# Kernel optimization log

Measured on AMD Instinct MI355X. Metric: run time of the kernel, lower is better.

The kernel has to match this reference:

```python
import jax, jax.numpy as jnp
import numpy as np
import math

B, L, D, H, NT, T, NLAYERS = 64, 128, 512, 8, 10000, 65536, 2
DH = D // H
FF = 2 * D
EPS = 1e-5


def setup_inputs() -> dict:
    key = jax.random.key(0)
    ks = jax.random.split(key, 20)
    item_ids = jax.random.randint(ks[0], (T,), 0, NT, dtype=jnp.int32)
    seg_ids = jnp.sort(jax.random.randint(ks[1], (T,), 0, B * L, dtype=jnp.int32))
    pad_mask = jnp.zeros((B, L), dtype=bool)
    future_mask = jnp.where(jnp.triu(jnp.ones((L, L), dtype=bool), k=1), -1e9, 0.0).astype(jnp.float32)

    s = 0.02
    emb = (jax.random.normal(ks[2], (NT + 1, D), jnp.float32) * s).at[NT].set(0.0)  # padding_idx row is zero
    Wqkv = jax.random.normal(ks[3], (NLAYERS, 3 * D, D), jnp.float32) * s
    bqkv = jnp.zeros((NLAYERS, 3 * D), jnp.float32)
    Wo = jax.random.normal(ks[4], (NLAYERS, D, D), jnp.float32) * s
    bo = jnp.zeros((NLAYERS, D), jnp.float32)
    W1 = jax.random.normal(ks[5], (NLAYERS, FF, D), jnp.float32) * s
    b1 = jnp.zeros((NLAYERS, FF), jnp.float32)
    W2 = jax.random.normal(ks[6], (NLAYERS, D, FF), jnp.float32) * s
    b2 = jnp.zeros((NLAYERS, D), jnp.float32)
    ln1_s = jnp.ones((NLAYERS, D), jnp.float32)
    ln1_b = jnp.zeros((NLAYERS, D), jnp.float32)
    ln2_s = jnp.ones((NLAYERS, D), jnp.float32)
    ln2_b = jnp.zeros((NLAYERS, D), jnp.float32)
    Wout = jax.random.normal(ks[7], (NT, D), jnp.float32) * s
    bout = jnp.zeros((NT,), jnp.float32)
    return dict(item_ids=item_ids, seg_ids=seg_ids, pad_mask=pad_mask, future_mask=future_mask,
                max_len=L, emb=emb, Wqkv=Wqkv, bqkv=bqkv, Wo=Wo, bo=bo, W1=W1, b1=b1, W2=W2, b2=b2,
                ln1_s=ln1_s, ln1_b=ln1_b, ln2_s=ln2_s, ln2_b=ln2_b, Wout=Wout, bout=bout)


def _layernorm(x, s, b):
    m = jnp.mean(x, axis=-1, keepdims=True)
    v = jnp.mean(jnp.square(x - m), axis=-1, keepdims=True)
    return (x - m) * jax.lax.rsqrt(v + EPS) * s + b


def _pos_encoding(maxlen, d):
    den = jnp.exp(-jnp.arange(0, d, 2, dtype=jnp.float32) * (math.log(10000.0) / d))
    pos = jnp.arange(maxlen, dtype=jnp.float32)[:, None]
    pe = jnp.zeros((maxlen, d), jnp.float32)
    pe = pe.at[:, 0::2].set(jnp.sin(pos * den))
    pe = pe.at[:, 1::2].set(jnp.cos(pos * den))
    return pe


def reference(item_ids, seg_ids, pad_mask, future_mask, max_len, emb,
              Wqkv, bqkv, Wo, bo, W1, b1, W2, b2, ln1_s, ln1_b, ln2_s, ln2_b, Wout, bout):
    # fused gather + segment-mean (replaces the per-user Python loops)
    counts = jax.ops.segment_sum(jnp.ones((T,), jnp.float32), seg_ids, num_segments=B * max_len)
    sums = jax.ops.segment_sum(emb[item_ids], seg_ids, num_segments=B * max_len)  # [B*L, D]
    means = jnp.where(counts[:, None] > 0, sums / jnp.maximum(counts, 1.0)[:, None], 0.0)
    x = means.reshape(B, max_len, D) + _pos_encoding(max_len, D)

    key_mask = jnp.where(pad_mask[:, None, None, :], -1e9, 0.0)  # [B,1,1,L]
    scale = 1.0 / math.sqrt(DH)
    for i in range(NLAYERS):
        qkv = x @ Wqkv[i].T + bqkv[i]                         # [B,L,3D]
        q, k, v = jnp.split(qkv, 3, axis=-1)
        q = q.reshape(B, max_len, H, DH)
        k = k.reshape(B, max_len, H, DH)
        v = v.reshape(B, max_len, H, DH)
        scores = jnp.einsum('bqhd,bkhd->bhqk', q, k) * scale + future_mask + key_mask
        attn = jax.nn.softmax(scores, axis=-1)
        o = jnp.einsum('bhqk,bkhd->bqhd', attn, v).reshape(B, max_len, D)
        o = o @ Wo[i].T + bo[i]
        x = _layernorm(x + o, ln1_s[i], ln1_b[i])              # post-norm
        ff = jax.nn.relu(x @ W1[i].T + b1[i]) @ W2[i].T + b2[i]
        x = _layernorm(x + ff, ln2_s[i], ln2_b[i])
    return x @ Wout.T + bout  # [B, L, num_types]
```

## Files before the change

kernel.cpp:

```cpp
#include <hip/hip_runtime.h>

#define T_TOTAL 65536
#define SEQ 128
#define DMODEL 512
#define DHEAD 64
#define NTYPES 10000
#define ROWS 8192
#define NOUT_PAD 10240

typedef float floatx4 __attribute__((ext_vector_type(4)));
typedef short shortx8 __attribute__((ext_vector_type(8)));

#define GLOAD_LDS(gp, lp) __builtin_amdgcn_global_load_lds( \
    (const __attribute__((address_space(1))) void*)(gp),    \
    (__attribute__((address_space(3))) void*)(lp), 16, 0, 0)

#define MFMA_BF16 __builtin_amdgcn_mfma_f32_16x16x32_bf16

__device__ __forceinline__ unsigned short f2bf(float f) {
  union { float f; unsigned u; } v; v.f = f;
  unsigned u = v.u + 0x7fffu + ((v.u >> 16) & 1u);
  return (unsigned short)(u >> 16);
}

__device__ __forceinline__ void phase_barrier() {
  __builtin_amdgcn_sched_barrier(0);
  __builtin_amdgcn_s_barrier();
  __builtin_amdgcn_sched_barrier(0);
}

__global__ __launch_bounds__(256) void convert_pad_kernel(
    const float* __restrict__ src, unsigned short* __restrict__ dst,
    long nsrc, long ndst) {
  long i = (long)blockIdx.x * 1024 + (long)threadIdx.x * 4;
  if (i >= ndst) return;
  float4 v = make_float4(0.f, 0.f, 0.f, 0.f);
  if (i < nsrc) v = *(const float4*)(src + i);
  ushort4 o;
  o.x = f2bf(v.x); o.y = f2bf(v.y); o.z = f2bf(v.z); o.w = f2bf(v.w);
  *(ushort4*)(dst + i) = o;
}

__global__ __launch_bounds__(128) void seg_mean_kernel(
    const int* __restrict__ item_ids, const int* __restrict__ seg_ids,
    const float* __restrict__ emb, float* __restrict__ x_f,
    unsigned short* __restrict__ x_b) {
  int s = blockIdx.x;
  int lo = 0, hi = T_TOTAL;
  while (lo < hi) { int mid = (lo + hi) >> 1; if (seg_ids[mid] < s) lo = mid + 1; else hi = mid; }
  int start = lo;
  hi = T_TOTAL;
  while (lo < hi) { int mid = (lo + hi) >> 1; if (seg_ids[mid] <= s) lo = mid + 1; else hi = mid; }
  int end = lo;
  int c = threadIdx.x << 2;
  float4 acc = make_float4(0.f, 0.f, 0.f, 0.f);
  for (int j = start; j < end; ++j) {
    const float* e = emb + (long)item_ids[j] * DMODEL + c;
    float4 v = *(const float4*)e;
    acc.x += v.x; acc.y += v.y; acc.z += v.z; acc.w += v.w;
  }
  int cnt = end - start;
  float inv = cnt > 0 ? 1.0f / (float)cnt : 0.0f;
  float mv[4] = {acc.x * inv, acc.y * inv, acc.z * inv, acc.w * inv};
  int l = s & (SEQ - 1);
  const float klog = 0.017988946039015984f;
  long base = (long)s * DMODEL + c;
#pragma unroll
  for (int t = 0; t < 4; ++t) {
    int col = c + t;
    float den = expf(-(float)(col & ~1) * klog);
    float ang = (float)l * den;
    float pe = (col & 1) ? cosf(ang) : sinf(ang);
    float val = mv[t] + pe;
    x_f[base + t] = val;
    x_b[base + t] = f2bf(val);
  }
}

__global__ __launch_bounds__(256) void gemm_bt_kernel(
    const unsigned short* __restrict__ A,
    const unsigned short* __restrict__ B,
    const float* __restrict__ bias,
    float* __restrict__ Cf,
    unsigned short* __restrict__ Cb,
    int K, int Nreal, int ldC, int relu) {
  __shared__ unsigned short As[128 * 32];
  __shared__ unsigned short Bs[128 * 32];
  const int tid = threadIdx.x;
  const int lane = tid & 63;
  const int wave = tid >> 6;
  const int wm = (wave >> 1) << 6;
  const int wn = (wave & 1) << 6;
  const int l16 = lane & 15;
  const int quad = lane >> 4;
  const long rowA0 = (long)blockIdx.x * 128;
  const long rowB0 = (long)blockIdx.y * 128;

  floatx4 acc[4][4] = {};

  const int rowOff = tid >> 2;
  const int kOff = (tid & 3) << 3;
  const unsigned short* gA = A + (rowA0 + rowOff) * (long)K + kOff;
  const unsigned short* gB = B + (rowB0 + rowOff) * (long)K + kOff;
  unsigned short* lA = As + tid * 8;
  unsigned short* lB = Bs + tid * 8;

  for (int k0 = 0; k0 < K; k0 += 32) {
    __syncthreads();
    GLOAD_LDS(gA + k0, lA);
    GLOAD_LDS(gA + 64 * (long)K + k0, lA + 2048);
    GLOAD_LDS(gB + k0, lB);
    GLOAD_LDS(gB + 64 * (long)K + k0, lB + 2048);
    __syncthreads();
    shortx8 af[4], bfr[4];
#pragma unroll
    for (int i = 0; i < 4; ++i)
      af[i] = *(const shortx8*)(As + (wm + i * 16 + l16) * 32 + quad * 8);
#pragma unroll
    for (int j = 0; j < 4; ++j)
      bfr[j] = *(const shortx8*)(Bs + (wn + j * 16 + l16) * 32 + quad * 8);
#pragma unroll
    for (int i = 0; i < 4; ++i)
#pragma unroll
      for (int j = 0; j < 4; ++j)
        acc[i][j] = MFMA_BF16(af[i], bfr[j], acc[i][j], 0, 0, 0);
  }

#pragma unroll
  for (int i = 0; i < 4; ++i) {
    int row = (int)rowA0 + wm + i * 16 + quad * 4;
#pragma unroll
    for (int j = 0; j < 4; ++j) {
      int col = (int)rowB0 + wn + j * 16 + l16;
      if (col < Nreal) {
        float bv = bias ? bias[col] : 0.0f;
#pragma unroll
        for (int r = 0; r < 4; ++r) {
          float v = acc[i][j][r] + bv;
          if (relu) v = fmaxf(v, 0.0f);
          long off = (long)(row + r) * ldC + col;
          if (Cf) Cf[off] = v;
          if (Cb) Cb[off] = f2bf(v);
        }
      }
    }
  }
}

__global__ __launch_bounds__(512, 2) void gemm256_kernel(
    const unsigned short* __restrict__ A,
    const unsigned short* __restrict__ B,
    const float* __restrict__ bias,
    float* __restrict__ Cf,
    unsigned short* __restrict__ Cb,
    int K, int Nreal, int ldC, int relu) {
  __shared__ unsigned short As[2][256 * 64];
  __shared__ unsigned short Bs[2][256 * 64];
  const int tid = threadIdx.x;
  const int lane = tid & 63;
  const int wave = tid >> 6;
  const int wm = wave >> 2;
  const int wn = wave & 3;
  const int l16 = lane & 15;
  const int quad = lane >> 4;
  const long rowA0 = (long)blockIdx.x * 256;
  const long rowB0 = (long)blockIdx.y * 256;

  floatx4 acc[8][4] = {};

  const int srow = tid >> 3;
  const int scol = (tid & 7) << 3;
  const unsigned short* gA = A + (rowA0 + srow) * (long)K + scol;
  const unsigned short* gB = B + (rowB0 + srow) * (long)K + scol;
  const int loff = tid * 8;
  const long rstep = 64 * (long)K;

#pragma unroll
  for (int is = 0; is < 4; ++is) {
    GLOAD_LDS(gA + is * rstep, &As[0][is * 4096 + loff]);
    GLOAD_LDS(gB + is * rstep, &Bs[0][is * 4096 + loff]);
  }
  asm volatile("s_waitcnt vmcnt(0)" ::: "memory");
  phase_barrier();

  const int KT = K >> 6;
  for (int kt = 0; kt < KT; ++kt) {
    const int cur = kt & 1;
    const unsigned short* Ab = As[cur];
    const unsigned short* Bb = Bs[cur];
    unsigned short* An = As[cur ^ 1];
    unsigned short* Bn = Bs[cur ^ 1];
    const bool stage = (kt + 1) < KT;
    const unsigned short* gAn = gA + (long)(kt + 1) * 64;
    const unsigned short* gBn = gB + (long)(kt + 1) * 64;

    shortx8 af[4][2], bf[4][2];

#pragma unroll
    for (int m = 0; m < 4; ++m) {
      const unsigned short* p = Ab + (wm * 128 + m * 16 + l16) * 64 + quad * 8;
      af[m][0] = *(const shortx8*)(p);
      af[m][1] = *(const shortx8*)(p + 32);
    }
#pragma unroll
    for (int n = 0; n < 2; ++n) {
      const unsigned short* p = Bb + (wn * 64 + n * 16 + l16) * 64 + quad * 8;
      bf[n][0] = *(const shortx8*)(p);
      bf[n][1] = *(const shortx8*)(p + 32);
    }
    if (stage) {
      GLOAD_LDS(gAn, An + loff);
      GLOAD_LDS(gAn + rstep, An + 4096 + loff);
    }
    phase_barrier();
    __builtin_amdgcn_s_setprio(1);
#pragma unroll
    for (int m = 0; m < 4; ++m)
#pragma unroll
      for (int n = 0; n < 2; ++n) {
        acc[m][n] = MFMA_BF16(af[m][0], bf[n][0], acc[m][n], 0, 0, 0);
        acc[m][n] = MFMA_BF16(af[m][1], bf[n][1], acc[m][n], 0, 0, 0);
      }
    __builtin_amdgcn_s_setprio(0);
    phase_barrier();

#pragma unroll
    for (int n = 2; n < 4; ++n) {
      const unsigned short* p = Bb + (wn * 64 + n * 16 + l16) * 64 + quad * 8;
      bf[n][0] = *(const shortx8*)(p);
      bf[n][1] = *(const shortx8*)(p + 32);
    }
    if (stage) {
      GLOAD_LDS(gAn + 2 * rstep, An + 8192 + loff);
      GLOAD_LDS(gAn + 3 * rstep, An + 12288 + loff);
    }
    phase_barrier();
    __builtin_amdgcn_s_setprio(1);
#pragma unroll
    for (int m = 0; m < 4; ++m)
#pragma unroll
      for (int n = 2; n < 4; ++n) {
        acc[m][n] = MFMA_BF16(af[m][0], bf[n][0], acc[m][n], 0, 0, 0);
        acc[m][n] = MFMA_BF16(af[m][1], bf[n][1], acc[m][n], 0, 0, 0);
      }
    __builtin_amdgcn_s_setprio(0);
    phase_barrier();

#pragma unroll
    for (int m = 0; m < 4; ++m) {
      const unsigned short* p = Ab + (wm * 128 + 64 + m * 16 + l16) * 64 + quad * 8;
      af[m][0] = *(const shortx8*)(p);
      af[m][1] = *(const shortx8*)(p + 32);
    }
    if (stage) {
      GLOAD_LDS(gBn, Bn + loff);
      GLOAD_LDS(gBn + rstep, Bn + 4096 + loff);
    }
    phase_barrier();
    __builtin_amdgcn_s_setprio(1);
#pragma unroll
    for (int m = 0; m < 4; ++m)
#pragma unroll
      for (int n = 0; n < 2; ++n) {
        acc[4 + m][n] = MFMA_BF16(af[m][0], bf[n][0], acc[4 + m][n], 0, 0, 0);
        acc[4 + m][n] = MFMA_BF16(af[m][1], bf[n][1], acc[4 + m][n], 0, 0, 0);
      }
    __builtin_amdgcn_s_setprio(0);
    phase_barrier();

    if (stage) {
      GLOAD_LDS(gBn + 2 * rstep, Bn + 8192 + loff);
      GLOAD_LDS(gBn + 3 * rstep, Bn + 12288 + loff);
    }
    phase_barrier();
    __builtin_amdgcn_s_setprio(1);
#pragma unroll
    for (int m = 0; m < 4; ++m)
#pragma unroll
      for (int n = 2; n < 4; ++n) {
        acc[4 + m][n] = MFMA_BF16(af[m][0], bf[n][0], acc[4 + m][n], 0, 0, 0);
        acc[4 + m][n] = MFMA_BF16(af[m][1], bf[n][1], acc[4 + m][n], 0, 0, 0);
      }
    __builtin_amdgcn_s_setprio(0);
    asm volatile("s_waitcnt vmcnt(0)" ::: "memory");
    phase_barrier();
  }

#pragma unroll
  for (int m = 0; m < 8; ++m) {
    int row = (int)rowA0 + wm * 128 + m * 16 + quad * 4;
#pragma unroll
    for (int n = 0; n < 4; ++n) {
      int col = (int)rowB0 + wn * 64 + n * 16 + l16;
      if (col < Nreal) {
        float bv = bias ? bias[col] : 0.0f;
#pragma unroll
        for (int r = 0; r < 4; ++r) {
          float v = acc[m][n][r] + bv;
          if (relu) v = fmaxf(v, 0.0f);
          long off = (long)(row + r) * ldC + col;
          if (Cf) Cf[off] = v;
          if (Cb) Cb[off] = f2bf(v);
        }
      }
    }
  }
}

__global__ __launch_bounds__(256) void attn_kernel(
    const float* __restrict__ qkv,
    unsigned short* __restrict__ o_b) {
  __shared__ float Ks[SEQ * DHEAD];
  __shared__ float Vs[SEQ * DHEAD];
  __shared__ float Ds[SEQ];
  int b = blockIdx.x >> 3, h = blockIdx.x & 7;
  const float* base = qkv + (long)b * SEQ * 1536;
  int hoff = h * DHEAD;
  for (int idx = threadIdx.x; idx < SEQ * DHEAD; idx += 256) {
    int l = idx >> 6, c = idx & 63;
    Ks[idx] = base[l * 1536 + 512 + hoff + c];
    Vs[idx] = base[l * 1536 + 1024 + hoff + c];
  }
  __syncthreads();
  int l = threadIdx.x & 127;
  int half = threadIdx.x >> 7;
  float q[DHEAD];
#pragma unroll
  for (int c = 0; c < DHEAD; ++c) q[c] = base[l * 1536 + hoff + c];
  float o[DHEAD];
#pragma unroll
  for (int c = 0; c < DHEAD; ++c) o[c] = 0.f;
  float denom = 0.f;
  for (int j = half; j <= l; j += 2) {
    const float* kr = Ks + j * DHEAD;
    float s0 = 0.f, s1 = 0.f, s2 = 0.f, s3 = 0.f;
#pragma unroll
    for (int c = 0; c < DHEAD; c += 4) {
      s0 += q[c] * kr[c];         s1 += q[c + 1] * kr[c + 1];
      s2 += q[c + 2] * kr[c + 2]; s3 += q[c + 3] * kr[c + 3];
    }
    float p = __expf(((s0 + s1) + (s2 + s3)) * 0.125f);
    denom += p;
    const float* vr = Vs + j * DHEAD;
#pragma unroll
    for (int c = 0; c < DHEAD; ++c) o[c] += p * vr[c];
  }
  __syncthreads();
  if (half) {
    float* os = Ks + l * DHEAD;
#pragma unroll
    for (int c = 0; c < DHEAD; ++c) os[c] = o[c];
    Ds[l] = denom;
  }
  __syncthreads();
  if (!half) {
    float dtot = denom + Ds[l];
    float inv = 1.0f / dtot;
    const float* os = Ks + l * DHEAD;
    unsigned short* dst = o_b + ((long)b * SEQ + l) * DMODEL + hoff;
#pragma unroll
    for (int c = 0; c < DHEAD; ++c) dst[c] = f2bf((o[c] + os[c]) * inv);
  }
}

__global__ __launch_bounds__(256) void add_ln_kernel(
    const float* __restrict__ x_in, const float* __restrict__ delta,
    const float* __restrict__ gamma, const float* __restrict__ beta,
    float* __restrict__ x_f, unsigned short* __restrict__ x_b) {
  int row = blockIdx.x;
  int tid = threadIdx.x;
  long base = (long)row * DMODEL;
  int c = tid * 2;
  float2 xv = *(const float2*)(x_in + base + c);
  float2 dv = *(const float2*)(delta + base + c);
  float a = xv.x + dv.x, b = xv.y + dv.y;
  float s = a + b;
  float sq = a * a + b * b;
#pragma unroll
  for (int off = 32; off > 0; off >>= 1) {
    s += __shfl_down(s, off, 64);
    sq += __shfl_down(sq, off, 64);
  }
  __shared__ float red[8];
  __shared__ float mean_s, rstd_s;
  int wv = tid >> 6, ln = tid & 63;
  if (ln == 0) { red[wv] = s; red[4 + wv] = sq; }
  __syncthreads();
  if (tid == 0) {
    float S = red[0] + red[1] + red[2] + red[3];
    float SQ = red[4] + red[5] + red[6] + red[7];
    float mean = S * (1.0f / 512.0f);
    float var = SQ * (1.0f / 512.0f) - mean * mean;
    mean_s = mean;
    rstd_s = rsqrtf(var + 1e-5f);
  }
  __syncthreads();
  float mean = mean_s, rstd = rstd_s;
  float o0 = (a - mean) * rstd * gamma[c] + beta[c];
  float o1 = (b - mean) * rstd * gamma[c + 1] + beta[c + 1];
  x_f[base + c] = o0;
  x_f[base + c + 1] = o1;
  x_b[base + c] = f2bf(o0);
  x_b[base + c + 1] = f2bf(o1);
}

extern "C" void kernel_launch(void* const* d_in, const int* in_sizes, int n_in,
                              void* d_out, int out_size, void* d_ws, size_t ws_size,
                              hipStream_t stream) {
  const int* item_ids = (const int*)d_in[0];
  const int* seg_ids = (const int*)d_in[1];
  const float* emb  = (const float*)d_in[5];
  const float* Wqkv = (const float*)d_in[6];
  const float* bqkv = (const float*)d_in[7];
  const float* Wo   = (const float*)d_in[8];
  const float* bo   = (const float*)d_in[9];
  const float* W1   = (const float*)d_in[10];
  const float* b1   = (const float*)d_in[11];
  const float* W2   = (const float*)d_in[12];
  const float* b2   = (const float*)d_in[13];
  const float* ln1s = (const float*)d_in[14];
  const float* ln1b = (const float*)d_in[15];
  const float* ln2s = (const float*)d_in[16];
  const float* ln2b = (const float*)d_in[17];
  const float* Wout = (const float*)d_in[18];
  const float* bout = (const float*)d_in[19];
  float* out = (float*)d_out;

  char* ws = (char*)d_ws;
  size_t off = 0;
  auto alloc = [&](size_t bytes) {
    void* p = ws + off;
    off += (bytes + 255) & ~(size_t)255;
    return p;
  };
  float* x_f  = (float*)alloc((size_t)ROWS * 512 * 4);
  unsigned short* x_b = (unsigned short*)alloc((size_t)ROWS * 512 * 2);
  float* qkv_f = (float*)alloc((size_t)ROWS * 1536 * 4);
  unsigned short* o_b = (unsigned short*)alloc((size_t)ROWS * 512 * 2);
  float* tmp_f = (float*)alloc((size_t)ROWS * 512 * 4);
  unsigned short* h_b = (unsigned short*)alloc((size_t)ROWS * 1024 * 2);
  unsigned short* wqkv_b = (unsigned short*)alloc((size_t)2 * 1536 * 512 * 2);
  unsigned short* wo_b = (unsigned short*)alloc((size_t)2 * 512 * 512 * 2);
  unsigned short* w1_b = (unsigned short*)alloc((size_t)2 * 1024 * 512 * 2);
  unsigned short* w2_b = (unsigned short*)alloc((size_t)2 * 512 * 1024 * 2);
  unsigned short* wout_b = (unsigned short*)alloc((size_t)NOUT_PAD * 512 * 2);

  auto cvt = [&](const float* src, unsigned short* dst, long nsrc, long ndst) {
    unsigned blocks = (unsigned)((ndst + 1023) / 1024);
    convert_pad_kernel<<<blocks, 256, 0, stream>>>(src, dst, nsrc, ndst);
  };
  cvt(Wqkv, wqkv_b, 2L * 1536 * 512, 2L * 1536 * 512);
  cvt(Wo, wo_b, 2L * 512 * 512, 2L * 512 * 512);
  cvt(W1, w1_b, 2L * 1024 * 512, 2L * 1024 * 512);
  cvt(W2, w2_b, 2L * 512 * 1024, 2L * 512 * 1024);
  cvt(Wout, wout_b, (long)NTYPES * 512, (long)NOUT_PAD * 512);

  seg_mean_kernel<<<ROWS, 128, 0, stream>>>(item_ids, seg_ids, emb, x_f, x_b);

  for (int i = 0; i < 2; ++i) {
    gemm256_kernel<<<dim3(32, 6), 512, 0, stream>>>(
        x_b, wqkv_b + (long)i * 1536 * 512, bqkv + i * 1536,
        qkv_f, nullptr, 512, 1536, 1536, 0);
    attn_kernel<<<512, 256, 0, stream>>>(qkv_f, o_b);
    gemm_bt_kernel<<<dim3(64, 4), 256, 0, stream>>>(
        o_b, wo_b + (long)i * 512 * 512, bo + i * 512,
        tmp_f, nullptr, 512, 512, 512, 0);
    add_ln_kernel<<<ROWS, 256, 0, stream>>>(x_f, tmp_f, ln1s + i * 512, ln1b + i * 512, x_f, x_b);
    gemm_bt_kernel<<<dim3(64, 8), 256, 0, stream>>>(
        x_b, w1_b + (long)i * 1024 * 512, b1 + i * 1024,
        nullptr, h_b, 512, 1024, 1024, 1);
    gemm_bt_kernel<<<dim3(64, 4), 256, 0, stream>>>(
        h_b, w2_b + (long)i * 512 * 1024, b2 + i * 512,
        tmp_f, nullptr, 1024, 512, 512, 0);
    add_ln_kernel<<<ROWS, 256, 0, stream>>>(x_f, tmp_f, ln2s + i * 512, ln2b + i * 512, x_f, x_b);
  }

  gemm256_kernel<<<dim3(32, 40), 512, 0, stream>>>(
      x_b, wout_b, bout, out, nullptr, 512, NTYPES, NTYPES, 0);
}
```

Baseline: 941.9 us.

## Fuse whole forward pass into one persistent cooperative megakernel with grid syncs

Replaces the sequence of separate launches (weight conversion, segment mean, GEMMs, attention, add+layernorm) with one cooperative persistent kernel of 256 blocks that loops over tiles and separates stages with grid-wide syncs. All GEMMs now use the 256x256 tile path, including the smaller ones that previously used 128x128 tiles. Add+layernorm is rewritten as a wave-per-row shuffle reduction with vectorized loads. The aim is to remove launch gaps and tail effects between the many small kernels, at the cost of grid-sync overhead, fewer tiles per GEMM for the small projections, and a fixed grid size that must fit co-resident.

```diff
diff --git a/kernel.cpp b/kernel.cpp
--- a/kernel.cpp
+++ b/kernel.cpp
@@ -1,4 +1,7 @@
 #include <hip/hip_runtime.h>
+#include <hip/hip_cooperative_groups.h>
+
+namespace cg = cooperative_groups;
 
 #define T_TOTAL 65536
 #define SEQ 128
@@ -7,6 +10,9 @@
 #define NTYPES 10000
 #define ROWS 8192
 #define NOUT_PAD 10240
+#define NBLOCKS 256
+#define NTHREADS 512
+#define SH_BYTES 132096
 
 typedef float floatx4 __attribute__((ext_vector_type(4)));
 typedef short shortx8 __attribute__((ext_vector_type(8)));
@@ -29,133 +35,88 @@
   __builtin_amdgcn_sched_barrier(0);
 }
 
-__global__ __launch_bounds__(256) void convert_pad_kernel(
-    const float* __restrict__ src, unsigned short* __restrict__ dst,
-    long nsrc, long ndst) {
-  long i = (long)blockIdx.x * 1024 + (long)threadIdx.x * 4;
-  if (i >= ndst) return;
-  float4 v = make_float4(0.f, 0.f, 0.f, 0.f);
-  if (i < nsrc) v = *(const float4*)(src + i);
-  ushort4 o;
-  o.x = f2bf(v.x); o.y = f2bf(v.y); o.z = f2bf(v.z); o.w = f2bf(v.w);
-  *(ushort4*)(dst + i) = o;
-}
-
-__global__ __launch_bounds__(128) void seg_mean_kernel(
-    const int* __restrict__ item_ids, const int* __restrict__ seg_ids,
-    const float* __restrict__ emb, float* __restrict__ x_f,
-    unsigned short* __restrict__ x_b) {
-  int s = blockIdx.x;
-  int lo = 0, hi = T_TOTAL;
-  while (lo < hi) { int mid = (lo + hi) >> 1; if (seg_ids[mid] < s) lo = mid + 1; else hi = mid; }
-  int start = lo;
-  hi = T_TOTAL;
-  while (lo < hi) { int mid = (lo + hi) >> 1; if (seg_ids[mid] <= s) lo = mid + 1; else hi = mid; }
-  int end = lo;
-  int c = threadIdx.x << 2;
-  float4 acc = make_float4(0.f, 0.f, 0.f, 0.f);
-  for (int j = start; j < end; ++j) {
-    const float* e = emb + (long)item_ids[j] * DMODEL + c;
-    float4 v = *(const float4*)e;
-    acc.x += v.x; acc.y += v.y; acc.z += v.z; acc.w += v.w;
-  }
-  int cnt = end - start;
-  float inv = cnt > 0 ? 1.0f / (float)cnt : 0.0f;
-  float mv[4] = {acc.x * inv, acc.y * inv, acc.z * inv, acc.w * inv};
-  int l = s & (SEQ - 1);
-  const float klog = 0.017988946039015984f;
-  long base = (long)s * DMODEL + c;
-#pragma unroll
-  for (int t = 0; t < 4; ++t) {
-    int col = c + t;
-    float den = expf(-(float)(col & ~1) * klog);
-    float ang = (float)l * den;
-    float pe = (col & 1) ? cosf(ang) : sinf(ang);
-    float val = mv[t] + pe;
-    x_f[base + t] = val;
-    x_b[base + t] = f2bf(val);
-  }
-}
-
-__global__ __launch_bounds__(256) void gemm_bt_kernel(
-    const unsigned short* __restrict__ A,
-    const unsigned short* __restrict__ B,
-    const float* __restrict__ bias,
-    float* __restrict__ Cf,
-    unsigned short* __restrict__ Cb,
-    int K, int Nreal, int ldC, int relu) {
-  __shared__ unsigned short As[128 * 32];
-  __shared__ unsigned short Bs[128 * 32];
-  const int tid = threadIdx.x;
-  const int lane = tid & 63;
-  const int wave = tid >> 6;
-  const int wm = (wave >> 1) << 6;
-  const int wn = (wave & 1) << 6;
-  const int l16 = lane & 15;
-  const int quad = lane >> 4;
-  const long rowA0 = (long)blockIdx.x * 128;
-  const long rowB0 = (long)blockIdx.y * 128;
-
-  floatx4 acc[4][4] = {};
-
-  const int rowOff = tid >> 2;
-  const int kOff = (tid & 3) << 3;
-  const unsigned short* gA = A + (rowA0 + rowOff) * (long)K + kOff;
-  const unsigned short* gB = B + (rowB0 + rowOff) * (long)K + kOff;
-  unsigned short* lA = As + tid * 8;
-  unsigned short* lB = Bs + tid * 8;
-
-  for (int k0 = 0; k0 < K; k0 += 32) {
-    __syncthreads();
-    GLOAD_LDS(gA + k0, lA);
-    GLOAD_LDS(gA + 64 * (long)K + k0, lA + 2048);
-    GLOAD_LDS(gB + k0, lB);
-    GLOAD_LDS(gB + 64 * (long)K + k0, lB + 2048);
-    __syncthreads();
-    shortx8 af[4], bfr[4];
-#pragma unroll
-    for (int i = 0; i < 4; ++i)
-      af[i] = *(const shortx8*)(As + (wm + i * 16 + l16) * 32 + quad * 8);
-#pragma unroll
-    for (int j = 0; j < 4; ++j)
-      bfr[j] = *(const shortx8*)(Bs + (wn + j * 16 + l16) * 32 + quad * 8);
-#pragma unroll
-    for (int i = 0; i < 4; ++i)
-#pragma unroll
-      for (int j = 0; j < 4; ++j)
-        acc[i][j] = MFMA_BF16(af[i], bfr[j], acc[i][j], 0, 0, 0);
-  }
-
-#pragma unroll
-  for (int i = 0; i < 4; ++i) {
-    int row = (int)rowA0 + wm + i * 16 + quad * 4;
-#pragma unroll
-    for (int j = 0; j < 4; ++j) {
-      int col = (int)rowB0 + wn + j * 16 + l16;
-      if (col < Nreal) {
-        float bv = bias ? bias[col] : 0.0f;
-#pragma unroll
-        for (int r = 0; r < 4; ++r) {
-          float v = acc[i][j][r] + bv;
-          if (relu) v = fmaxf(v, 0.0f);
-          long off = (long)(row + r) * ldC + col;
-          if (Cf) Cf[off] = v;
-          if (Cb) Cb[off] = f2bf(v);
-        }
-      }
-    }
-  }
-}
-
-__global__ __launch_bounds__(512, 2) void gemm256_kernel(
-    const unsigned short* __restrict__ A,
-    const unsigned short* __restrict__ B,
-    const float* __restrict__ bias,
-    float* __restrict__ Cf,
-    unsigned short* __restrict__ Cb,
-    int K, int Nreal, int ldC, int relu) {
-  __shared__ unsigned short As[2][256 * 64];
-  __shared__ unsigned short Bs[2][256 * 64];
+struct MegaParams {
+  const int* item_ids; const int* seg_ids;
+  const float* emb;
+  const float* bqkv; const float* bo; const float* b1; const float* b2;
+  const float* ln1s; const float* ln1b; const float* ln2s; const float* ln2b;
+  const float* bout;
+  const float* Wqkv; const float* Wo; const float* W1; const float* W2; const float* Wout;
+  float* out;
+  float* x_f; unsigned short* x_b; float* qkv_f; unsigned short* o_b;
+  float* tmp_f; unsigned short* h_b;
+  unsigned short* wqkv_b; unsigned short* wo_b; unsigned short* w1_b;
+  unsigned short* w2_b; unsigned short* wout_b;
+};
+
+__device__ __forceinline__ void dev_converts(const MegaParams& P) {
+  const long Q0 = 1572864L / 4;
+  const long Q1 = Q0 + 524288L / 4;
+  const long Q2 = Q1 + 1048576L / 4;
+  const long Q3 = Q2 + 1048576L / 4;
+  const long Q4 = Q3 + 5242880L / 4;
+  const long stride = (long)NBLOCKS * NTHREADS;
+  for (long q = (long)blockIdx.x * NTHREADS + threadIdx.x; q < Q4; q += stride) {
+    const float* src; unsigned short* dst; long i; bool guard = false;
+    if (q < Q0)      { src = P.Wqkv; dst = P.wqkv_b; i = q; }
+    else if (q < Q1) { src = P.Wo;   dst = P.wo_b;   i = q - Q0; }
+    else if (q < Q2) { src = P.W1;   dst = P.w1_b;   i = q - Q1; }
+    else if (q < Q3) { src = P.W2;   dst = P.w2_b;   i = q - Q2; }
+    else             { src = P.Wout; dst = P.wout_b; i = q - Q3; guard = true; }
+    long e = i * 4;
+    float4 v = make_float4(0.f, 0.f, 0.f, 0.f);
+    if (!guard || e < 5120000L) v = *(const float4*)(src + e);
+    ushort4 o;
+    o.x = f2bf(v.x); o.y = f2bf(v.y); o.z = f2bf(v.z); o.w = f2bf(v.w);
+    *(ushort4*)(dst + e) = o;
+  }
+}
+
+__device__ __forceinline__ void dev_seg_mean(const MegaParams& P) {
+  int g = threadIdx.x >> 7;
+  int t128 = threadIdx.x & 127;
+  int c = t128 << 2;
+#pragma unroll
+  for (int it = 0; it < 8; ++it) {
+    int s = blockIdx.x * 32 + it * 4 + g;
+    int lo = 0, hi = T_TOTAL;
+    while (lo < hi) { int mid = (lo + hi) >> 1; if (P.seg_ids[mid] < s) lo = mid + 1; else hi = mid; }
+    int start = lo;
+    hi = T_TOTAL;
+    while (lo < hi) { int mid = (lo + hi) >> 1; if (P.seg_ids[mid] <= s) lo = mid + 1; else hi = mid; }
+    int end = lo;
+    float4 acc = make_float4(0.f, 0.f, 0.f, 0.f);
+    for (int j = start; j < end; ++j) {
+      const float* e = P.emb + (long)P.item_ids[j] * DMODEL + c;
+      float4 v = *(const float4*)e;
+      acc.x += v.x; acc.y += v.y; acc.z += v.z; acc.w += v.w;
+    }
+    int cnt = end - start;
+    float inv = cnt > 0 ? 1.0f / (float)cnt : 0.0f;
+    float mv[4] = {acc.x * inv, acc.y * inv, acc.z * inv, acc.w * inv};
+    int l = s & (SEQ - 1);
+    const float klog = 0.017988946039015984f;
+    long base = (long)s * DMODEL + c;
+#pragma unroll
+    for (int t = 0; t < 4; ++t) {
+      int col = c + t;
+      float den = expf(-(float)(col & ~1) * klog);
+      float ang = (float)l * den;
+      float pe = (col & 1) ? cosf(ang) : sinf(ang);
+      float val = mv[t] + pe;
+      P.x_f[base + t] = val;
+      P.x_b[base + t] = f2bf(val);
+    }
+  }
+}
+
+__device__ __forceinline__ void dev_gemm(char* sh,
+    const unsigned short* __restrict__ A, const unsigned short* __restrict__ B,
+    const float* __restrict__ bias, float* __restrict__ Cf,
+    unsigned short* __restrict__ Cb, int K, int Nreal, int ldC, int relu,
+    int tilesX, int tilesY) {
+  unsigned short* AsBase = (unsigned short*)sh;
+  unsigned short* BsBase = (unsigned short*)(sh + 65536);
   const int tid = threadIdx.x;
   const int lane = tid & 63;
   const int wave = tid >> 6;
@@ -163,167 +124,167 @@
   const int wn = wave & 3;
   const int l16 = lane & 15;
   const int quad = lane >> 4;
-  const long rowA0 = (long)blockIdx.x * 256;
-  const long rowB0 = (long)blockIdx.y * 256;
-
-  floatx4 acc[8][4] = {};
-
   const int srow = tid >> 3;
   const int scol = (tid & 7) << 3;
-  const unsigned short* gA = A + (rowA0 + srow) * (long)K + scol;
-  const unsigned short* gB = B + (rowB0 + srow) * (long)K + scol;
   const int loff = tid * 8;
   const long rstep = 64 * (long)K;
-
-#pragma unroll
-  for (int is = 0; is < 4; ++is) {
-    GLOAD_LDS(gA + is * rstep, &As[0][is * 4096 + loff]);
-    GLOAD_LDS(gB + is * rstep, &Bs[0][is * 4096 + loff]);
-  }
-  asm volatile("s_waitcnt vmcnt(0)" ::: "memory");
-  phase_barrier();
-
+  const int nt = tilesX * tilesY;
   const int KT = K >> 6;
-  for (int kt = 0; kt < KT; ++kt) {
-    const int cur = kt & 1;
-    const unsigned short* Ab = As[cur];
-    const unsigned short* Bb = Bs[cur];
-    unsigned short* An = As[cur ^ 1];
-    unsigned short* Bn = Bs[cur ^ 1];
-    const bool stage = (kt + 1) < KT;
-    const unsigned short* gAn = gA + (long)(kt + 1) * 64;
-    const unsigned short* gBn = gB + (long)(kt + 1) * 64;
-
-    shortx8 af[4][2], bf[4][2];
-
-#pragma unroll
-    for (int m = 0; m < 4; ++m) {
-      const unsigned short* p = Ab + (wm * 128 + m * 16 + l16) * 64 + quad * 8;
-      af[m][0] = *(const shortx8*)(p);
-      af[m][1] = *(const shortx8*)(p + 32);
-    }
-#pragma unroll
-    for (int n = 0; n < 2; ++n) {
-      const unsigned short* p = Bb + (wn * 64 + n * 16 + l16) * 64 + quad * 8;
-      bf[n][0] = *(const shortx8*)(p);
-      bf[n][1] = *(const shortx8*)(p + 32);
-    }
-    if (stage) {
-      GLOAD_LDS(gAn, An + loff);
-      GLOAD_LDS(gAn + rstep, An + 4096 + loff);
-    }
-    phase_barrier();
-    __builtin_amdgcn_s_setprio(1);
-#pragma unroll
-    for (int m = 0; m < 4; ++m)
-#pragma unroll
-      for (int n = 0; n < 2; ++n) {
-        acc[m][n] = MFMA_BF16(af[m][0], bf[n][0], acc[m][n], 0, 0, 0);
-        acc[m][n] = MFMA_BF16(af[m][1], bf[n][1], acc[m][n], 0, 0, 0);
-      }
-    __builtin_amdgcn_s_setprio(0);
-    phase_barrier();
-
-#pragma unroll
-    for (int n = 2; n < 4; ++n) {
-      const unsigned short* p = Bb + (wn * 64 + n * 16 + l16) * 64 + quad * 8;
-      bf[n][0] = *(const shortx8*)(p);
-      bf[n][1] = *(const shortx8*)(p + 32);
-    }
-    if (stage) {
-      GLOAD_LDS(gAn + 2 * rstep, An + 8192 + loff);
-      GLOAD_LDS(gAn + 3 * rstep, An + 12288 + loff);
-    }
-    phase_barrier();
-    __builtin_amdgcn_s_setprio(1);
-#pragma unroll
-    for (int m = 0; m < 4; ++m)
-#pragma unroll
-      for (int n = 2; n < 4; ++n) {
-        acc[m][n] = MFMA_BF16(af[m][0], bf[n][0], acc[m][n], 0, 0, 0);
-        acc[m][n] = MFMA_BF16(af[m][1], bf[n][1], acc[m][n], 0, 0, 0);
-      }
-    __builtin_amdgcn_s_setprio(0);
-    phase_barrier();
-
-#pragma unroll
-    for (int m = 0; m < 4; ++m) {
-      const unsigned short* p = Ab + (wm * 128 + 64 + m * 16 + l16) * 64 + quad * 8;
-      af[m][0] = *(const shortx8*)(p);
-      af[m][1] = *(const shortx8*)(p + 32);
-    }
-    if (stage) {
-      GLOAD_LDS(gBn, Bn + loff);
-      GLOAD_LDS(gBn + rstep, Bn + 4096 + loff);
-    }
-    phase_barrier();
-    __builtin_amdgcn_s_setprio(1);
-#pragma unroll
-    for (int m = 0; m < 4; ++m)
-#pragma unroll
-      for (int n = 0; n < 2; ++n) {
-        acc[4 + m][n] = MFMA_BF16(af[m][0], bf[n][0], acc[4 + m][n], 0, 0, 0);
-        acc[4 + m][n] = MFMA_BF16(af[m][1], bf[n][1], acc[4 + m][n], 0, 0, 0);
-      }
-    __builtin_amdgcn_s_setprio(0);
-    phase_barrier();
-
-    if (stage) {
-      GLOAD_LDS(gBn + 2 * rstep, Bn + 8192 + loff);
-      GLOAD_LDS(gBn + 3 * rstep, Bn + 12288 + loff);
-    }
-    phase_barrier();
-    __builtin_amdgcn_s_setprio(1);
-#pragma unroll
-    for (int m = 0; m < 4; ++m)
-#pragma unroll
-      for (int n = 2; n < 4; ++n) {
-        acc[4 + m][n] = MFMA_BF16(af[m][0], bf[n][0], acc[4 + m][n], 0, 0, 0);
-        acc[4 + m][n] = MFMA_BF16(af[m][1], bf[n][1], acc[4 + m][n], 0, 0, 0);
-      }
-    __builtin_amdgcn_s_setprio(0);
+
+  for (int t = blockIdx.x; t < nt; t += NBLOCKS) {
+    int tbx = t % tilesX, tby = t / tilesX;
+    long rowA0 = (long)tbx * 256;
+    long rowB0 = (long)tby * 256;
+    floatx4 acc[8][4] = {};
+    const unsigned short* gA = A + (rowA0 + srow) * (long)K + scol;
+    const unsigned short* gB = B + (rowB0 + srow) * (long)K + scol;
+
+#pragma unroll
+    for (int is = 0; is < 4; ++is) {
+      GLOAD_LDS(gA + is * rstep, AsBase + is * 4096 + loff);
+      GLOAD_LDS(gB + is * rstep, BsBase + is * 4096 + loff);
+    }
     asm volatile("s_waitcnt vmcnt(0)" ::: "memory");
     phase_barrier();
-  }
-
-#pragma unroll
-  for (int m = 0; m < 8; ++m) {
-    int row = (int)rowA0 + wm * 128 + m * 16 + quad * 4;
-#pragma unroll
-    for (int n = 0; n < 4; ++n) {
-      int col = (int)rowB0 + wn * 64 + n * 16 + l16;
-      if (col < Nreal) {
-        float bv = bias ? bias[col] : 0.0f;
-#pragma unroll
-        for (int r = 0; r < 4; ++r) {
-          float v = acc[m][n][r] + bv;
-          if (relu) v = fmaxf(v, 0.0f);
-          long off = (long)(row + r) * ldC + col;
-          if (Cf) Cf[off] = v;
-          if (Cb) Cb[off] = f2bf(v);
+
+    for (int kt = 0; kt < KT; ++kt) {
+      const int cur = kt & 1;
+      const unsigned short* Ab = AsBase + cur * 16384;
+      const unsigned short* Bb = BsBase + cur * 16384;
+      unsigned short* An = AsBase + (cur ^ 1) * 16384;
+      unsigned short* Bn = BsBase + (cur ^ 1) * 16384;
+      const bool stage = (kt + 1) < KT;
+      const unsigned short* gAn = gA + (long)(kt + 1) * 64;
+      const unsigned short* gBn = gB + (long)(kt + 1) * 64;
+
+      shortx8 af[4][2], bf[4][2];
+
+#pragma unroll
+      for (int m = 0; m < 4; ++m) {
+        const unsigned short* p = Ab + (wm * 128 + m * 16 + l16) * 64 + quad * 8;
+        af[m][0] = *(const shortx8*)(p);
+        af[m][1] = *(const shortx8*)(p + 32);
+      }
+#pragma unroll
+      for (int n = 0; n < 2; ++n) {
+        const unsigned short* p = Bb + (wn * 64 + n * 16 + l16) * 64 + quad * 8;
+        bf[n][0] = *(const shortx8*)(p);
+        bf[n][1] = *(const shortx8*)(p + 32);
+      }
+      if (stage) {
+        GLOAD_LDS(gAn, An + loff);
+        GLOAD_LDS(gAn + rstep, An + 4096 + loff);
+        GLOAD_LDS(gAn + 2 * rstep, An + 8192 + loff);
+        GLOAD_LDS(gAn + 3 * rstep, An + 12288 + loff);
+      }
+      phase_barrier();
+      __builtin_amdgcn_s_setprio(1);
+#pragma unroll
+      for (int m = 0; m < 4; ++m)
+#pragma unroll
+        for (int n = 0; n < 2; ++n) {
+          acc[m][n] = MFMA_BF16(af[m][0], bf[n][0], acc[m][n], 0, 0, 0);
+          acc[m][n] = MFMA_BF16(af[m][1], bf[n][1], acc[m][n], 0, 0, 0);
         }
-      }
-    }
-  }
-}
-
-__global__ __launch_bounds__(256) void attn_kernel(
-    const float* __restrict__ qkv,
-    unsigned short* __restrict__ o_b) {
-  __shared__ float Ks[SEQ * DHEAD];
-  __shared__ float Vs[SEQ * DHEAD];
-  __shared__ float Ds[SEQ];
-  int b = blockIdx.x >> 3, h = blockIdx.x & 7;
+      __builtin_amdgcn_s_setprio(0);
+      phase_barrier();
+
+#pragma unroll
+      for (int n = 2; n < 4; ++n) {
+        const unsigned short* p = Bb + (wn * 64 + n * 16 + l16) * 64 + quad * 8;
+        bf[n][0] = *(const shortx8*)(p);
+        bf[n][1] = *(const shortx8*)(p + 32);
+      }
+      if (stage) {
+        GLOAD_LDS(gBn, Bn + loff);
+        GLOAD_LDS(gBn + rstep, Bn + 4096 + loff);
+        GLOAD_LDS(gBn + 2 * rstep, Bn + 8192 + loff);
+        GLOAD_LDS(gBn + 3 * rstep, Bn + 12288 + loff);
+      }
+      phase_barrier();
+      __builtin_amdgcn_s_setprio(1);
+#pragma unroll
+      for (int m = 0; m < 4; ++m)
+#pragma unroll
+        for (int n = 2; n < 4; ++n) {
+          acc[m][n] = MFMA_BF16(af[m][0], bf[n][0], acc[m][n], 0, 0, 0);
+          acc[m][n] = MFMA_BF16(af[m][1], bf[n][1], acc[m][n], 0, 0, 0);
+        }
+      __builtin_amdgcn_s_setprio(0);
+      phase_barrier();
+
+#pragma unroll
+      for (int m = 0; m < 4; ++m) {
+        const unsigned short* p = Ab + (wm * 128 + 64 + m * 16 + l16) * 64 + quad * 8;
+        af[m][0] = *(const shortx8*)(p);
+        af[m][1] = *(const shortx8*)(p + 32);
+      }
+      phase_barrier();
+      __builtin_amdgcn_s_setprio(1);
+#pragma unroll
+      for (int m = 0; m < 4; ++m)
+#pragma unroll
+        for (int n = 0; n < 2; ++n) {
+          acc[4 + m][n] = MFMA_BF16(af[m][0], bf[n][0], acc[4 + m][n], 0, 0, 0);
+          acc[4 + m][n] = MFMA_BF16(af[m][1], bf[n][1], acc[4 + m][n], 0, 0, 0);
+        }
+      __builtin_amdgcn_s_setprio(0);
+      phase_barrier();
+
+      __builtin_amdgcn_s_setprio(1);
+#pragma unroll
+      for (int m = 0; m < 4; ++m)
+#pragma unroll
+        for (int n = 2; n < 4; ++n) {
+          acc[4 + m][n] = MFMA_BF16(af[m][0], bf[n][0], acc[4 + m][n], 0, 0, 0);
+          acc[4 + m][n] = MFMA_BF16(af[m][1], bf[n][1], acc[4 + m][n], 0, 0, 0);
+        }
+      __builtin_amdgcn_s_setprio(0);
+      asm volatile("s_waitcnt vmcnt(0)" ::: "memory");
+      phase_barrier();
+    }
+
+#pragma unroll
+    for (int m = 0; m < 8; ++m) {
+      int row = (int)rowA0 + wm * 128 + m * 16 + quad * 4;
+#pragma unroll
+      for (int n = 0; n < 4; ++n) {
+        int col = (int)rowB0 + wn * 64 + n * 16 + l16;
+        if (col < Nreal) {
+          float bv = bias ? bias[col] : 0.0f;
+#pragma unroll
+          for (int r = 0; r < 4; ++r) {
+            float v = acc[m][n][r] + bv;
+            if (relu) v = fmaxf(v, 0.0f);
+            long off = (long)(row + r) * ldC + col;
+            if (Cf) Cf[off] = v;
+            if (Cb) Cb[off] = f2bf(v);
+          }
+        }
+      }
+    }
+  }
+}
+
+__device__ __forceinline__ void dev_attn(char* sh, const float* __restrict__ qkv,
+                                         unsigned short* __restrict__ o_b) {
+  const int ph = threadIdx.x >> 8;
+  const int t256 = threadIdx.x & 255;
+  float* Ks = (float*)sh + ph * 8192;
+  float* Vs = (float*)(sh + 65536) + ph * 8192;
+  float* Ds = (float*)(sh + 131072) + ph * 128;
+  int p = blockIdx.x * 2 + ph;
+  int b = p >> 3, h = p & 7;
   const float* base = qkv + (long)b * SEQ * 1536;
   int hoff = h * DHEAD;
-  for (int idx = threadIdx.x; idx < SEQ * DHEAD; idx += 256) {
+  for (int idx = t256; idx < SEQ * DHEAD; idx += 256) {
     int l = idx >> 6, c = idx & 63;
     Ks[idx] = base[l * 1536 + 512 + hoff + c];
     Vs[idx] = base[l * 1536 + 1024 + hoff + c];
   }
   __syncthreads();
-  int l = threadIdx.x & 127;
-  int half = threadIdx.x >> 7;
+  int l = t256 & 127;
+  int half = t256 >> 7;
   float q[DHEAD];
 #pragma unroll
   for (int c = 0; c < DHEAD; ++c) q[c] = base[l * 1536 + hoff + c];
@@ -339,11 +300,11 @@
       s0 += q[c] * kr[c];         s1 += q[c + 1] * kr[c + 1];
       s2 += q[c + 2] * kr[c + 2]; s3 += q[c + 3] * kr[c + 3];
     }
-    float p = __expf(((s0 + s1) + (s2 + s3)) * 0.125f);
-    denom += p;
+    float pv = __expf(((s0 + s1) + (s2 + s3)) * 0.125f);
+    denom += pv;
     const float* vr = Vs + j * DHEAD;
 #pragma unroll
-    for (int c = 0; c < DHEAD; ++c) o[c] += p * vr[c];
+    for (int c = 0; c < DHEAD; ++c) o[c] += pv * vr[c];
   }
   __syncthreads();
   if (half) {
@@ -363,69 +324,81 @@
   }
 }
 
-__global__ __launch_bounds__(256) void add_ln_kernel(
-    const float* __restrict__ x_in, const float* __restrict__ delta,
-    const float* __restrict__ gamma, const float* __restrict__ beta,
-    float* __restrict__ x_f, unsigned short* __restrict__ x_b) {
-  int row = blockIdx.x;
-  int tid = threadIdx.x;
-  long base = (long)row * DMODEL;
-  int c = tid * 2;
-  float2 xv = *(const float2*)(x_in + base + c);
-  float2 dv = *(const float2*)(delta + base + c);
-  float a = xv.x + dv.x, b = xv.y + dv.y;
-  float s = a + b;
-  float sq = a * a + b * b;
-#pragma unroll
-  for (int off = 32; off > 0; off >>= 1) {
-    s += __shfl_down(s, off, 64);
-    sq += __shfl_down(sq, off, 64);
-  }
-  __shared__ float red[8];
-  __shared__ float mean_s, rstd_s;
-  int wv = tid >> 6, ln = tid & 63;
-  if (ln == 0) { red[wv] = s; red[4 + wv] = sq; }
-  __syncthreads();
-  if (tid == 0) {
-    float S = red[0] + red[1] + red[2] + red[3];
-    float SQ = red[4] + red[5] + red[6] + red[7];
-    float mean = S * (1.0f / 512.0f);
-    float var = SQ * (1.0f / 512.0f) - mean * mean;
-    mean_s = mean;
-    rstd_s = rsqrtf(var + 1e-5f);
-  }
-  __syncthreads();
-  float mean = mean_s, rstd = rstd_s;
-  float o0 = (a - mean) * rstd * gamma[c] + beta[c];
-  float o1 = (b - mean) * rstd * gamma[c + 1] + beta[c + 1];
-  x_f[base + c] = o0;
-  x_f[base + c + 1] = o1;
-  x_b[base + c] = f2bf(o0);
-  x_b[base + c + 1] = f2bf(o1);
+__device__ __forceinline__ void dev_add_ln(const float* __restrict__ x_in,
+    const float* __restrict__ delta, const float* __restrict__ gamma,
+    const float* __restrict__ beta, float* __restrict__ x_f,
+    unsigned short* __restrict__ x_b) {
+  int w = threadIdx.x >> 6, lane = threadIdx.x & 63;
+  int c = lane * 8;
+#pragma unroll
+  for (int it = 0; it < 4; ++it) {
+    int row = blockIdx.x * 32 + it * 8 + w;
+    long base = (long)row * DMODEL;
+    float4 v0 = *(const float4*)(x_in + base + c);
+    float4 v1 = *(const float4*)(x_in + base + c + 4);
+    float4 d0 = *(const float4*)(delta + base + c);
+    float4 d1 = *(const float4*)(delta + base + c + 4);
+    float e[8] = {v0.x + d0.x, v0.y + d0.y, v0.z + d0.z, v0.w + d0.w,
+                  v1.x + d1.x, v1.y + d1.y, v1.z + d1.z, v1.w + d1.w};
+    float s = 0.f, sq = 0.f;
+#pragma unroll
+    for (int k = 0; k < 8; ++k) { s += e[k]; sq += e[k] * e[k]; }
+#pragma unroll
+    for (int off = 1; off < 64; off <<= 1) {
+      s += __shfl_xor(s, off, 64);
+      sq += __shfl_xor(sq, off, 64);
+    }
+    float mean = s * (1.0f / 512.0f);
+    float var = sq * (1.0f / 512.0f) - mean * mean;
+    float rstd = rsqrtf(var + 1e-5f);
+    float of[8]; unsigned short ob[8];
+#pragma unroll
+    for (int k = 0; k < 8; ++k) {
+      float o = (e[k] - mean) * rstd * gamma[c + k] + beta[c + k];
+      of[k] = o; ob[k] = f2bf(o);
+    }
+    *(float4*)(x_f + base + c) = make_float4(of[0], of[1], of[2], of[3]);
+    *(float4*)(x_f + base + c + 4) = make_float4(of[4], of[5], of[6], of[7]);
+    *(ushort4*)(x_b + base + c) = make_ushort4(ob[0], ob[1], ob[2], ob[3]);
+    *(ushort4*)(x_b + base + c + 4) = make_ushort4(ob[4], ob[5], ob[6], ob[7]);
+  }
+}
+
+__global__ __launch_bounds__(NTHREADS, 2) void mega_kernel(MegaParams P) {
+  __shared__ __attribute__((aligned(128))) char sh[SH_BYTES];
+  cg::grid_group grid = cg::this_grid();
+
+  dev_converts(P);
+  dev_seg_mean(P);
+  grid.sync();
+
+  for (int i = 0; i < 2; ++i) {
+    dev_gemm(sh, P.x_b, P.wqkv_b + (long)i * 1536 * 512, P.bqkv + i * 1536,
+             P.qkv_f, nullptr, 512, 1536, 1536, 0, 32, 6);
+    grid.sync();
+    dev_attn(sh, P.qkv_f, P.o_b);
+    grid.sync();
+    dev_gemm(sh, P.o_b, P.wo_b + (long)i * 512 * 512, P.bo + i * 512,
+             P.tmp_f, nullptr, 512, 512, 512, 0, 32, 2);
+    grid.sync();
+    dev_add_ln(P.x_f, P.tmp_f, P.ln1s + i * 512, P.ln1b + i * 512, P.x_f, P.x_b);
+    grid.sync();
+    dev_gemm(sh, P.x_b, P.w1_b + (long)i * 1024 * 512, P.b1 + i * 1024,
+             nullptr, P.h_b, 512, 1024, 1024, 1, 32, 4);
+    grid.sync();
+    dev_gemm(sh, P.h_b, P.w2_b + (long)i * 512 * 1024, P.b2 + i * 512,
+             P.tmp_f, nullptr, 1024, 512, 512, 0, 32, 2);
+    grid.sync();
+    dev_add_ln(P.x_f, P.tmp_f, P.ln2s + i * 512, P.ln2b + i * 512, P.x_f, P.x_b);
+    grid.sync();
+  }
+
+  dev_gemm(sh, P.x_b, P.wout_b, P.bout, P.out, nullptr, 512, NTYPES, NTYPES, 0, 32, 40);
 }
 
 extern "C" void kernel_launch(void* const* d_in, const int* in_sizes, int n_in,
                               void* d_out, int out_size, void* d_ws, size_t ws_size,
                               hipStream_t stream) {
-  const int* item_ids = (const int*)d_in[0];
-  const int* seg_ids = (const int*)d_in[1];
-  const float* emb  = (const float*)d_in[5];
-  const float* Wqkv = (const float*)d_in[6];
-  const float* bqkv = (const float*)d_in[7];
-  const float* Wo   = (const float*)d_in[8];
-  const float* bo   = (const float*)d_in[9];
-  const float* W1   = (const float*)d_in[10];
-  const float* b1   = (const float*)d_in[11];
-  const float* W2   = (const float*)d_in[12];
-  const float* b2   = (const float*)d_in[13];
-  const float* ln1s = (const float*)d_in[14];
-  const float* ln1b = (const float*)d_in[15];
-  const float* ln2s = (const float*)d_in[16];
-  const float* ln2b = (const float*)d_in[17];
-  const float* Wout = (const float*)d_in[18];
-  const float* bout = (const float*)d_in[19];
-  float* out = (float*)d_out;
-
   char* ws = (char*)d_ws;
   size_t off = 0;
   auto alloc = [&](size_t bytes) {
@@ -433,48 +406,40 @@
     off += (bytes + 255) & ~(size_t)255;
     return p;
   };
-  float* x_f  = (float*)alloc((size_t)ROWS * 512 * 4);
-  unsigned short* x_b = (unsigned short*)alloc((size_t)ROWS * 512 * 2);
-  float* qkv_f = (float*)alloc((size_t)ROWS * 1536 * 4);
-  unsigned short* o_b = (unsigned short*)alloc((size_t)ROWS * 512 * 2);
-  float* tmp_f = (float*)alloc((size_t)ROWS * 512 * 4);
-  unsigned short* h_b = (unsigned short*)alloc((size_t)ROWS * 1024 * 2);
-  unsigned short* wqkv_b = (unsigned short*)alloc((size_t)2 * 1536 * 512 * 2);
-  unsigned short* wo_b = (unsigned short*)alloc((size_t)2 * 512 * 512 * 2);
-  unsigned short* w1_b = (unsigned short*)alloc((size_t)2 * 1024 * 512 * 2);
-  unsigned short* w2_b = (unsigned short*)alloc((size_t)2 * 512 * 1024 * 2);
-  unsigned short* wout_b = (unsigned short*)alloc((size_t)NOUT_PAD * 512 * 2);
-
-  auto cvt = [&](const float* src, unsigned short* dst, long nsrc, long ndst) {
-    unsigned blocks = (unsigned)((ndst + 1023) / 1024);
-    convert_pad_kernel<<<blocks, 256, 0, stream>>>(src, dst, nsrc, ndst);
-  };
-  cvt(Wqkv, wqkv_b, 2L * 1536 * 512, 2L * 1536 * 512);
-  cvt(Wo, wo_b, 2L * 512 * 512, 2L * 512 * 512);
-  cvt(W1, w1_b, 2L * 1024 * 512, 2L * 1024 * 512);
-  cvt(W2, w2_b, 2L * 512 * 1024, 2L * 512 * 1024);
-  cvt(Wout, wout_b, (long)NTYPES * 512, (long)NOUT_PAD * 512);
-
-  seg_mean_kernel<<<ROWS, 128, 0, stream>>>(item_ids, seg_ids, emb, x_f, x_b);
-
-  for (int i = 0; i < 2; ++i) {
-    gemm256_kernel<<<dim3(32, 6), 512, 0, stream>>>(
-        x_b, wqkv_b + (long)i * 1536 * 512, bqkv + i * 1536,
-        qkv_f, nullptr, 512, 1536, 1536, 0);
-    attn_kernel<<<512, 256, 0, stream>>>(qkv_f, o_b);
-    gemm_bt_kernel<<<dim3(64, 4), 256, 0, stream>>>(
-        o_b, wo_b + (long)i * 512 * 512, bo + i * 512,
-        tmp_f, nullptr, 512, 512, 512, 0);
-    add_ln_kernel<<<ROWS, 256, 0, stream>>>(x_f, tmp_f, ln1s + i * 512, ln1b + i * 512, x_f, x_b);
-    gemm_bt_kernel<<<dim3(64, 8), 256, 0, stream>>>(
-        x_b, w1_b + (long)i * 1024 * 512, b1 + i * 1024,
-        nullptr, h_b, 512, 1024, 1024, 1);
-    gemm_bt_kernel<<<dim3(64, 4), 256, 0, stream>>>(
-        h_b, w2_b + (long)i * 512 * 1024, b2 + i * 512,
-        tmp_f, nullptr, 1024, 512, 512, 0);
-    add_ln_kernel<<<ROWS, 256, 0, stream>>>(x_f, tmp_f, ln2s + i * 512, ln2b + i * 512, x_f, x_b);
-  }
-
-  gemm256_kernel<<<dim3(32, 40), 512, 0, stream>>>(
-      x_b, wout_b, bout, out, nullptr, 512, NTYPES, NTYPES, 0);
-}
+
+  MegaParams P;
+  P.item_ids = (const int*)d_in[0];
+  P.seg_ids  = (const int*)d_in[1];
+  P.emb  = (const float*)d_in[5];
+  P.Wqkv = (const float*)d_in[6];
+  P.bqkv = (const float*)d_in[7];
+  P.Wo   = (const float*)d_in[8];
+  P.bo   = (const float*)d_in[9];
+  P.W1   = (const float*)d_in[10];
+  P.b1   = (const float*)d_in[11];
+  P.W2   = (const float*)d_in[12];
+  P.b2   = (const float*)d_in[13];
+  P.ln1s = (const float*)d_in[14];
+  P.ln1b = (const float*)d_in[15];
+  P.ln2s = (const float*)d_in[16];
+  P.ln2b = (const float*)d_in[17];
+  P.Wout = (const float*)d_in[18];
+  P.bout = (const float*)d_in[19];
+  P.out  = (float*)d_out;
+
+  P.x_f    = (float*)alloc((size_t)ROWS * 512 * 4);
+  P.x_b    = (unsigned short*)alloc((size_t)ROWS * 512 * 2);
+  P.qkv_f  = (float*)alloc((size_t)ROWS * 1536 * 4);
+  P.o_b    = (unsigned short*)alloc((size_t)ROWS * 512 * 2);
+  P.tmp_f  = (float*)alloc((size_t)ROWS * 512 * 4);
+  P.h_b    = (unsigned short*)alloc((size_t)ROWS * 1024 * 2);
+  P.wqkv_b = (unsigned short*)alloc((size_t)2 * 1536 * 512 * 2);
+  P.wo_b   = (unsigned short*)alloc((size_t)2 * 512 * 512 * 2);
+  P.w1_b   = (unsigned short*)alloc((size_t)2 * 1024 * 512 * 2);
+  P.w2_b   = (unsigned short*)alloc((size_t)2 * 512 * 1024 * 2);
+  P.wout_b = (unsigned short*)alloc((size_t)NOUT_PAD * 512 * 2);
+
+  void* args[] = {(void*)&P};
+  hipLaunchCooperativeKernel((void*)mega_kernel, dim3(NBLOCKS), dim3(NTHREADS),
+                             args, 0, stream);
+}
```

New measurement: 1.619 ms. 71.9% more time.
